# Kernel tuning notes

Hardware: AMD Instinct MI355X
Metric: run time of the kernel (lower is better)

## Reference

```python
import jax, jax.numpy as jnp
import numpy as np

VOCAB = 32000
HID = 1024
HEADS = 16
HEAD_DIM = HID // HEADS
LAYERS = 8
INTER = 4 * HID
ROPE_BASE = 100000.0
EPS = 1e-5


def setup_inputs() -> dict:
    key = jax.random.key(0)
    ks = jax.random.split(key, 12)
    s = 0.02
    inp = {
        'input_ids': jax.random.randint(ks[0], (2, 2048), 0, VOCAB),
        'embed_W': jax.random.normal(ks[1], (VOCAB, HID), jnp.float32) * s,
        'Wq': jax.random.normal(ks[2], (LAYERS, HID, HID), jnp.float32) * s,
        'Wk': jax.random.normal(ks[3], (LAYERS, HID, HID), jnp.float32) * s,
        'Wv': jax.random.normal(ks[4], (LAYERS, HID, HID), jnp.float32) * s,
        'Wo': jax.random.normal(ks[5], (LAYERS, HID, HID), jnp.float32) * s,
        'Wg': jax.random.normal(ks[6], (LAYERS, HID, INTER), jnp.float32) * s,
        'Wu': jax.random.normal(ks[7], (LAYERS, HID, INTER), jnp.float32) * s,
        'Wd': jax.random.normal(ks[8], (LAYERS, INTER, HID), jnp.float32) * s,
        'norm1_w': jnp.ones((LAYERS, HID), jnp.float32),
        'norm2_w': jnp.ones((LAYERS, HID), jnp.float32),
        'final_norm_w': jnp.ones((HID,), jnp.float32),
        'head_W': jax.random.normal(ks[9], (HID, VOCAB), jnp.float32) * s,
    }
    return inp


def rms_norm(x, w):
    return x * jax.lax.rsqrt(jnp.mean(x * x, axis=-1, keepdims=True) + EPS) * w


def rope_tables(seq_len):
    freq = 1.0 / (ROPE_BASE ** (jnp.arange(0, HEAD_DIM, 2, dtype=jnp.float32) / HEAD_DIM))
    ang = jnp.arange(seq_len, dtype=jnp.float32)[:, None] * freq  # [S, d/2]
    cos = jnp.concatenate([jnp.cos(ang), jnp.cos(ang)], axis=-1)  # [S, d]
    sin = jnp.concatenate([jnp.sin(ang), jnp.sin(ang)], axis=-1)
    return cos, sin


def rotate_half(x):
    h = x.shape[-1] // 2
    return jnp.concatenate([-x[..., h:], x[..., :h]], axis=-1)


def apply_rope(q, k, cos, sin):
    # q,k: [B,S,H,D]; cos,sin: [S,D] -> broadcast over heads via [:,None,:]
    c = cos[:, None, :]
    s = sin[:, None, :]
    return q * c + rotate_half(q) * s, k * c + rotate_half(k) * s


def attention(x, wq, wk, wv, wo, cos, sin, causal_mask):
    B, S, _ = x.shape
    q = (x @ wq).reshape(B, S, HEADS, HEAD_DIM)
    k = (x @ wk).reshape(B, S, HEADS, HEAD_DIM)
    v = (x @ wv).reshape(B, S, HEADS, HEAD_DIM)
    q, k = apply_rope(q, k, cos, sin)
    scores = jnp.einsum('bqhd,bkhd->bhqk', q, k) / np.sqrt(HEAD_DIM)
    scores = jnp.clip(scores, -1000.0, 1000.0)
    scores = jnp.where(causal_mask, jnp.finfo(scores.dtype).min, scores)
    w = jax.nn.softmax(scores.astype(jnp.float32), axis=-1).astype(q.dtype)
    w = jnp.clip(w, 0.0, 1.0)
    ctx = jnp.einsum('bhqk,bkhd->bqhd', w, v).reshape(B, S, HID)
    return ctx @ wo


def reference(input_ids, embed_W, Wq, Wk, Wv, Wo, Wg, Wu, Wd, norm1_w, norm2_w, final_norm_w, head_W):
    B, S = input_ids.shape
    h = embed_W[input_ids]  # [B,S,HID]
    cos, sin = rope_tables(S)
    causal_mask = jnp.triu(jnp.ones((S, S), bool), k=1)[None, None]
    for l in range(LAYERS):
        h = h + attention(rms_norm(h, norm1_w[l]), Wq[l], Wk[l], Wv[l], Wo[l], cos, sin, causal_mask)
        hn = rms_norm(h, norm2_w[l])
        h = h + (jax.nn.silu(hn @ Wg[l]) * (hn @ Wu[l])) @ Wd[l]
    h = rms_norm(h, final_norm_w)
    logits = h @ head_W
    return logits, h
```

## Files before the change

kernel.cpp:

```cpp
#include <hip/hip_runtime.h>

#define T_TOK 4096
#define SEQ   2048
#define HID   1024
#define NH    16
#define HD    64
#define INTER 4096
#define NLAYER 8
#define VOCAB 32000

typedef short short8 __attribute__((ext_vector_type(8)));
typedef float f32x4  __attribute__((ext_vector_type(4)));

__device__ __forceinline__ unsigned short f2bf(float f){
  unsigned int u = __builtin_bit_cast(unsigned int, f);
  u += 0x7fffu + ((u >> 16) & 1u);
  return (unsigned short)(u >> 16);
}
__device__ __forceinline__ float bf2f(unsigned short b){
  unsigned int u = ((unsigned int)b) << 16;
  return __builtin_bit_cast(float, u);
}

#define GLOAD_LDS16(gsrc, ldst) \
  __builtin_amdgcn_global_load_lds((const __attribute__((address_space(1))) void*)(gsrc), \
                                   (__attribute__((address_space(3))) void*)(ldst), 16, 0, 0)

__global__ __launch_bounds__(256) void embed_kernel(const int* __restrict__ ids,
                                                    const float* __restrict__ W,
                                                    float* __restrict__ h){
  int i = blockIdx.x * 256 + threadIdx.x;
  int t = i >> 8, c = i & 255;
  ((float4*)h)[i] = ((const float4*)(W + (size_t)ids[t] * HID))[c];
}

__global__ __launch_bounds__(256) void rope_tab_kernel(float* __restrict__ cosT,
                                                       float* __restrict__ sinT){
  int i = blockIdx.x * 256 + threadIdx.x;
  int s = i >> 5, f = i & 31;
  float inv = expf(-((2.0f * (float)f) / 64.0f) * logf(100000.0f));
  float ang = (float)s * inv;
  cosT[i] = cosf(ang);
  sinT[i] = sinf(ang);
}

__global__ __launch_bounds__(256) void rmsnorm_kernel(const float* __restrict__ h,
                                                      const float* __restrict__ w,
                                                      unsigned short* __restrict__ out,
                                                      float* hcopy){
  int t = blockIdx.x, tid = threadIdx.x;
  float4 v = ((const float4*)(h + (size_t)t * HID))[tid];
  float ss = v.x*v.x + v.y*v.y + v.z*v.z + v.w*v.w;
  #pragma unroll
  for (int m = 1; m < 64; m <<= 1) ss += __shfl_xor(ss, m);
  __shared__ float red[4];
  if ((tid & 63) == 0) red[tid >> 6] = ss;
  __syncthreads();
  float r = rsqrtf((red[0] + red[1] + red[2] + red[3]) * (1.0f / HID) + 1e-5f);
  float4 wv = ((const float4*)w)[tid];
  float nx = v.x * r * wv.x;
  float ny = v.y * r * wv.y;
  float nz = v.z * r * wv.z;
  float nw = v.w * r * wv.w;
  ushort4 o;
  o.x = f2bf(nx); o.y = f2bf(ny); o.z = f2bf(nz); o.w = f2bf(nw);
  ((ushort4*)(out + (size_t)t * HID))[tid] = o;
  if (hcopy){
    float4 hv; hv.x = nx; hv.y = ny; hv.z = nz; hv.w = nw;
    ((float4*)(hcopy + (size_t)t * HID))[tid] = hv;
  }
}

__global__ __launch_bounds__(256) void convert_w_swz(const float* __restrict__ W,
                                                     unsigned short* __restrict__ Wt,
                                                     int K, int N){
  __shared__ unsigned short t_lds[64][72];
  W  += (size_t)blockIdx.z * K * N;
  Wt += (size_t)blockIdx.z * K * N;
  const int n0 = blockIdx.x * 64, k0 = blockIdx.y * 64;
  const int tid = threadIdx.x;
  const int tr = tid >> 4, tc = tid & 15;
  #pragma unroll
  for (int i = 0; i < 4; ++i){
    int kk = tr + i * 16;
    float4 v = *(const float4*)(W + (size_t)(k0 + kk) * N + n0 + tc * 4);
    t_lds[tc*4+0][kk] = f2bf(v.x);
    t_lds[tc*4+1][kk] = f2bf(v.y);
    t_lds[tc*4+2][kk] = f2bf(v.z);
    t_lds[tc*4+3][kk] = f2bf(v.w);
  }
  __syncthreads();
  const int n = tid >> 2, cp = tid & 3;
  #pragma unroll
  for (int j = 0; j < 2; ++j){
    int c = cp * 2 + j;
    uint4 d = *(const uint4*)(&t_lds[n][c * 8]);
    *(uint4*)(Wt + (size_t)(n0 + n) * K + k0 + ((c ^ (n & 7)) << 3)) = d;
  }
}

__global__ __launch_bounds__(256) void convert_w_lin(const float* __restrict__ W,
                                                     unsigned short* __restrict__ Wt,
                                                     int K, int N){
  __shared__ unsigned short t_lds[64][72];
  const int n0 = blockIdx.x * 64, k0 = blockIdx.y * 64;
  const int tid = threadIdx.x;
  const int tr = tid >> 4, tc = tid & 15;
  #pragma unroll
  for (int i = 0; i < 4; ++i){
    int kk = tr + i * 16;
    float4 v = *(const float4*)(W + (size_t)(k0 + kk) * N + n0 + tc * 4);
    t_lds[tc*4+0][kk] = f2bf(v.x);
    t_lds[tc*4+1][kk] = f2bf(v.y);
    t_lds[tc*4+2][kk] = f2bf(v.z);
    t_lds[tc*4+3][kk] = f2bf(v.w);
  }
  __syncthreads();
  const int n = tid >> 2, cp = tid & 3;
  #pragma unroll
  for (int j = 0; j < 2; ++j){
    int c = cp * 2 + j;
    uint4 d = *(const uint4*)(&t_lds[n][c * 8]);
    *(uint4*)(Wt + (size_t)(n0 + n) * K + k0 + c * 8) = d;
  }
}

__device__ __forceinline__ void gemm_core64(const unsigned short* __restrict__ A,
                                            const unsigned short* __restrict__ Bt,
                                            int K, int m0, int n0,
                                            unsigned short* As, unsigned short* Bs,
                                            f32x4 (&acc)[4][4]){
  const int tid = threadIdx.x;
  const int lane = tid & 63, w = tid >> 6;
  const int l15 = lane & 15, g = lane >> 4;
  const int lr = lane >> 3;
  const int lc = lane & 7;
  const int wr = w >> 1, wc = w & 1;
  const int axor = ((lc ^ lr) << 3);

  #pragma unroll
  for (int m = 0; m < 4; ++m)
    #pragma unroll
    for (int n = 0; n < 4; ++n)
      #pragma unroll
      for (int i = 0; i < 4; ++i) acc[m][n][i] = 0.0f;

  for (int kk = 0; kk < K; kk += 64){
    __syncthreads();
    #pragma unroll
    for (int i = 0; i < 4; ++i){
      int rb = (i * 4 + w) * 8;
      GLOAD_LDS16(A  + (size_t)(m0 + rb + lr) * K + kk + axor,      As + rb * 64);
      GLOAD_LDS16(Bt + (size_t)(n0 + rb + lr) * K + kk + (lc << 3), Bs + rb * 64);
    }
    __syncthreads();
    short8 a[4][2], b[4][2];
    const int x = l15 & 7;
    #pragma unroll
    for (int m = 0; m < 4; ++m){
      int row = wr * 64 + m * 16 + l15;
      a[m][0] = *(const short8*)(As + row * 64 + ((g       ^ x) << 3));
      a[m][1] = *(const short8*)(As + row * 64 + (((4 + g) ^ x) << 3));
    }
    #pragma unroll
    for (int n = 0; n < 4; ++n){
      int row = wc * 64 + n * 16 + l15;
      b[n][0] = *(const short8*)(Bs + row * 64 + ((g       ^ x) << 3));
      b[n][1] = *(const short8*)(Bs + row * 64 + (((4 + g) ^ x) << 3));
    }
    #pragma unroll
    for (int m = 0; m < 4; ++m)
      #pragma unroll
      for (int n = 0; n < 4; ++n){
        acc[m][n] = __builtin_amdgcn_mfma_f32_16x16x32_bf16(a[m][0], b[n][0], acc[m][n], 0, 0, 0);
        acc[m][n] = __builtin_amdgcn_mfma_f32_16x16x32_bf16(a[m][1], b[n][1], acc[m][n], 0, 0, 0);
      }
  }
}

__device__ __forceinline__ void gemm_core32(const unsigned short* __restrict__ A,
                                            const unsigned short* __restrict__ Bt,
                                            int K, int m0, int n0,
                                            unsigned short* As, unsigned short* Bs,
                                            f32x4 (&acc)[4][4]){
  const int tid = threadIdx.x;
  const int lane = tid & 63, w = tid >> 6;
  const int l15 = lane & 15, g = lane >> 4;
  const int wr = w >> 1, wc = w & 1;
  const int srow = lane >> 2;
  const int schunk = (((lane & 3) ^ ((srow >> 1) & 3)) << 3);
  const int sx = (l15 >> 1) & 3;

  #pragma unroll
  for (int m = 0; m < 4; ++m)
    #pragma unroll
    for (int n = 0; n < 4; ++n)
      #pragma unroll
      for (int i = 0; i < 4; ++i) acc[m][n][i] = 0.0f;

  for (int kk = 0; kk < K; kk += 32){
    __syncthreads();
    GLOAD_LDS16(A  + (size_t)(m0 +      w*16 + srow) * K + kk + schunk, As + (w*16) * 32);
    GLOAD_LDS16(A  + (size_t)(m0 + 64 + w*16 + srow) * K + kk + schunk, As + (64 + w*16) * 32);
    GLOAD_LDS16(Bt + (size_t)(n0 +      w*16 + srow) * K + kk + schunk, Bs + (w*16) * 32);
    GLOAD_LDS16(Bt + (size_t)(n0 + 64 + w*16 + srow) * K + kk + schunk, Bs + (64 + w*16) * 32);
    __syncthreads();
    short8 a[4], b[4];
    #pragma unroll
    for (int m = 0; m < 4; ++m)
      a[m] = *(const short8*)(As + (wr*64 + m*16 + l15) * 32 + ((g ^ sx) << 3));
    #pragma unroll
    for (int n = 0; n < 4; ++n)
      b[n] = *(const short8*)(Bs + (wc*64 + n*16 + l15) * 32 + ((g ^ sx) << 3));
    #pragma unroll
    for (int m = 0; m < 4; ++m)
      #pragma unroll
      for (int n = 0; n < 4; ++n)
        acc[m][n] = __builtin_amdgcn_mfma_f32_16x16x32_bf16(a[m], b[n], acc[m][n], 0, 0, 0);
  }
}

template<int MODE>
__device__ __forceinline__ void gemm_epi(const f32x4 (&acc)[4][4], void* Cout,
                                         const float* __restrict__ resid,
                                         int N, int m0, int n0, int ldt){
  const int tid = threadIdx.x;
  const int lane = tid & 63, w = tid >> 6;
  const int l15 = lane & 15, g = lane >> 4;
  const int wr = w >> 1, wc = w & 1;
  #pragma unroll
  for (int m = 0; m < 4; ++m){
    #pragma unroll
    for (int n = 0; n < 4; ++n){
      int row0 = m0 + wr * 64 + m * 16 + g * 4;
      int col  = n0 + wc * 64 + n * 16 + l15;
      #pragma unroll
      for (int i = 0; i < 4; ++i){
        float v = acc[m][n][i];
        if (MODE == 0){
          ((unsigned short*)Cout)[(size_t)(row0 + i) * N + col] = f2bf(v);
        } else if (MODE == 1){
          size_t idx = (size_t)(row0 + i) * N + col;
          ((float*)Cout)[idx] = resid[idx] + v;
        } else if (MODE == 2){
          ((unsigned short*)Cout)[(size_t)col * ldt + (row0 + i)] = f2bf(v);
        } else {
          __builtin_nontemporal_store(v, &((float*)Cout)[(size_t)(row0 + i) * N + col]);
        }
      }
    }
  }
}

template<int MODE>
__global__ __launch_bounds__(256) void gemm64_k(const unsigned short* __restrict__ A,
                                                const unsigned short* __restrict__ Bt,
                                                void* Cout, const float* resid,
                                                int K, int N, int ldt){
  __shared__ unsigned short As[128 * 64];
  __shared__ unsigned short Bs[128 * 64];
  f32x4 acc[4][4];
  gemm_core64(A, Bt, K, blockIdx.x * 128, blockIdx.y * 128, As, Bs, acc);
  gemm_epi<MODE>(acc, Cout, resid, N, blockIdx.x * 128, blockIdx.y * 128, ldt);
}

template<int MODE>
__global__ __launch_bounds__(256) void gemm32_k(const unsigned short* __restrict__ A,
                                                const unsigned short* __restrict__ Bt,
                                                void* Cout, const float* resid,
                                                int K, int N, int ldt){
  __shared__ unsigned short As[128 * 32];
  __shared__ unsigned short Bs[128 * 32];
  f32x4 acc[4][4];
  gemm_core32(A, Bt, K, blockIdx.x * 128, blockIdx.y * 128, As, Bs, acc);
  gemm_epi<MODE>(acc, Cout, resid, N, blockIdx.x * 128, blockIdx.y * 128, ldt);
}

__global__ __launch_bounds__(256) void gemm_qkv(const unsigned short* __restrict__ A,
                                                const unsigned short* __restrict__ BtQ,
                                                const unsigned short* __restrict__ BtK,
                                                const unsigned short* __restrict__ BtV,
                                                unsigned short* qb, unsigned short* kb,
                                                unsigned short* vt,
                                                const float* __restrict__ cosT,
                                                const float* __restrict__ sinT){
  __shared__ unsigned short As[128 * 64];
  __shared__ unsigned short Bs[128 * 64];
  const int nb = blockIdx.y, sel = nb >> 3, n0 = (nb & 7) * 128;
  const unsigned short* Bt = (sel == 0) ? BtQ : (sel == 1) ? BtK : BtV;
  f32x4 acc[4][4];
  gemm_core64(A, Bt, HID, blockIdx.x * 128, n0, As, Bs, acc);
  if (sel == 2){
    gemm_epi<2>(acc, vt, nullptr, HID, blockIdx.x * 128, n0, T_TOK);
    return;
  }
  unsigned short* outp = sel ? kb : qb;
  const float qs = sel ? 1.0f : 0.125f;
  const int tid = threadIdx.x;
  const int lane = tid & 63, w = tid >> 6;
  const int l15 = lane & 15, g = lane >> 4;
  const int wr = w >> 1, wc = w & 1;
  const int m0 = blockIdx.x * 128;
  #pragma unroll
  for (int m = 0; m < 4; ++m){
    #pragma unroll
    for (int n = 0; n < 2; ++n){
      int row0 = m0 + wr * 64 + m * 16 + g * 4;
      int col  = n0 + wc * 64 + n * 16 + l15;
      int f    = (col & 63);
      #pragma unroll
      for (int i = 0; i < 4; ++i){
        int t = row0 + i, s = t & (SEQ - 1);
        float c  = cosT[s * 32 + f];
        float sn = sinT[s * 32 + f];
        float x0 = acc[m][n][i], x1 = acc[m][n + 2][i];
        outp[(size_t)t * HID + col]      = f2bf((x0 * c - x1 * sn) * qs);
        outp[(size_t)t * HID + col + 32] = f2bf((x1 * c + x0 * sn) * qs);
      }
    }
  }
}

__global__ __launch_bounds__(256) void gemm_gu(const unsigned short* __restrict__ A,
                                               const unsigned short* __restrict__ BtG,
                                               const unsigned short* __restrict__ BtU,
                                               unsigned short* gb, unsigned short* ub){
  __shared__ unsigned short As[128 * 64];
  __shared__ unsigned short Bs[128 * 64];
  const int nb = blockIdx.y, sel = nb >> 5, n0 = (nb & 31) * 128;
  f32x4 acc[4][4];
  gemm_core64(A, sel ? BtU : BtG, HID, blockIdx.x * 128, n0, As, Bs, acc);
  gemm_epi<0>(acc, sel ? ub : gb, nullptr, INTER, blockIdx.x * 128, n0, 0);
}

__global__ __launch_bounds__(256, 2) void gemm_f32b(const unsigned short* __restrict__ A,
                                                    const float* __restrict__ Bw,
                                                    float* __restrict__ Cout,
                                                    int M, int N, int K){
  __shared__ unsigned short As[128 * 32];
  __shared__ unsigned short Bs[128 * 32];
  const int tid = threadIdx.x;
  const int lane = tid & 63, wid = tid >> 6;
  const int l15 = lane & 15, g = lane >> 4;
  const int wr = wid >> 1, wc = wid & 1;
  const int m0 = blockIdx.x * 128, n0 = blockIdx.y * 128;
  const int bcol = tid & 127, bhalf = tid >> 7;
  f32x4 acc[4][4];
  #pragma unroll
  for (int m = 0; m < 4; ++m)
    #pragma unroll
    for (int n = 0; n < 4; ++n)
      #pragma unroll
      for (int i = 0; i < 4; ++i) acc[m][n][i] = 0.0f;
  for (int kk = 0; kk < K; kk += 32){
    __syncthreads();
    #pragma unroll
    for (int cc = 0; cc < 2; ++cc){
      int c = tid + cc * 256;
      int row = c >> 2, kc = (c & 3) << 3;
      uint4 d = *(const uint4*)(A + (size_t)(m0 + row) * K + kk + kc);
      *(uint4*)(&As[row * 32 + kc]) = d;
    }
    {
      const float* bp = Bw + (size_t)(kk + bhalf * 16) * N + n0 + bcol;
      float f[16];
      #pragma unroll
      for (int j = 0; j < 16; ++j) f[j] = bp[(size_t)j * N];
      unsigned int pk[8];
      #pragma unroll
      for (int j = 0; j < 8; ++j)
        pk[j] = (unsigned int)f2bf(f[2*j]) | ((unsigned int)f2bf(f[2*j+1]) << 16);
      int sw = (bcol >> 1) & 3;
      int c0 = ((bhalf << 1)     ) ^ sw;
      int c1 = ((bhalf << 1) | 1 ) ^ sw;
      uint4 w0; w0.x = pk[0]; w0.y = pk[1]; w0.z = pk[2]; w0.w = pk[3];
      uint4 w1; w1.x = pk[4]; w1.y = pk[5]; w1.z = pk[6]; w1.w = pk[7];
      *(uint4*)(&Bs[bcol * 32 + c0 * 8]) = w0;
      *(uint4*)(&Bs[bcol * 32 + c1 * 8]) = w1;
    }
    __syncthreads();
    short8 a[4], b[4];
    #pragma unroll
    for (int m = 0; m < 4; ++m)
      a[m] = *(const short8*)(&As[(wr*64 + m*16 + l15) * 32 + g*8]);
    #pragma unroll
    for (int n = 0; n < 4; ++n){
      int col = wc*64 + n*16 + l15;
      b[n] = *(const short8*)(&Bs[col * 32 + (g ^ ((col >> 1) & 3)) * 8]);
    }
    #pragma unroll
    for (int m = 0; m < 4; ++m)
      #pragma unroll
      for (int n = 0; n < 4; ++n)
        acc[m][n] = __builtin_amdgcn_mfma_f32_16x16x32_bf16(a[m], b[n], acc[m][n], 0, 0, 0);
  }
  #pragma unroll
  for (int m = 0; m < 4; ++m)
    #pragma unroll
    for (int n = 0; n < 4; ++n){
      int row0 = m0 + wr*64 + m*16 + g*4;
      int col  = n0 + wc*64 + n*16 + l15;
      #pragma unroll
      for (int i = 0; i < 4; ++i)
        Cout[(size_t)(row0 + i) * N + col] = acc[m][n][i];
    }
}

__global__ __launch_bounds__(512) void attn_kernel(const unsigned short* __restrict__ q,
                                                   const unsigned short* __restrict__ k,
                                                   const unsigned short* __restrict__ vt,
                                                   unsigned short* __restrict__ ctx){
  const int tid = threadIdx.x;
  const int lane = tid & 63, w = tid >> 6;
  const int l15 = lane & 15, g = lane >> 4;
  const int bx = (int)gridDim.x - 1 - (int)blockIdx.x;
  const int q0 = bx * 128 + w * 16;
  const int hh = blockIdx.y;
  const int tb = blockIdx.z * SEQ;

  __shared__ unsigned short Ks[64][72];
  __shared__ unsigned short Vs[64][72];
  __shared__ unsigned short Ps[8][16][72];

  short8 qa[2];
  #pragma unroll
  for (int kd = 0; kd < 2; ++kd)
    qa[kd] = *(const short8*)(q + (size_t)(tb + q0 + l15) * HID + hh*HD + kd*32 + g*8);

  float m_run[4], l_run[4];
  f32x4 o_acc[4];
  #pragma unroll
  for (int i = 0; i < 4; ++i){ m_run[i] = -1e30f; l_run[i] = 0.0f; }
  #pragma unroll
  for (int dt = 0; dt < 4; ++dt)
    #pragma unroll
    for (int i = 0; i < 4; ++i) o_acc[dt][i] = 0.0f;

  const int ntile = 2 * bx + 2;
  const int srow = tid >> 3, sc = (tid & 7) * 8;
  const unsigned short* kbase = k  + (size_t)(tb + srow) * HID + hh*HD + sc;
  const unsigned short* vbase = vt + (size_t)(hh*HD + srow) * T_TOK + tb + sc;

  for (int kt = 0; kt < ntile; ++kt){
    const int kv0 = kt * 64;
    __syncthreads();
    *(uint4*)(&Ks[srow][sc]) = *(const uint4*)(kbase + (size_t)kv0 * HID);
    *(uint4*)(&Vs[srow][sc]) = *(const uint4*)(vbase + kv0);
    __syncthreads();
    const int dq = q0 + 15 - kv0;
    const int nct = (dq < 0) ? 0 : min(4, (dq >> 4) + 1);
    if (nct <= 0) continue;

    float pv[4][4];
    #pragma unroll
    for (int ct = 0; ct < 4; ++ct){
      if (ct < nct){
        f32x4 scv;
        #pragma unroll
        for (int i = 0; i < 4; ++i) scv[i] = 0.0f;
        scv = __builtin_amdgcn_mfma_f32_16x16x32_bf16(qa[0],
                *(const short8*)(&Ks[ct*16 + l15][g*8]), scv, 0, 0, 0);
        scv = __builtin_amdgcn_mfma_f32_16x16x32_bf16(qa[1],
                *(const short8*)(&Ks[ct*16 + l15][32 + g*8]), scv, 0, 0, 0);
        #pragma unroll
        for (int i = 0; i < 4; ++i){
          float s = fminf(fmaxf(scv[i], -1000.0f), 1000.0f);
          int row = q0 + g*4 + i;
          int col = kv0 + ct*16 + l15;
          pv[ct][i] = (col > row) ? -1e30f : s;
        }
      } else {
        #pragma unroll
        for (int i = 0; i < 4; ++i) pv[ct][i] = -1e30f;
      }
    }
    #pragma unroll
    for (int i = 0; i < 4; ++i){
      float mx = fmaxf(fmaxf(pv[0][i], pv[1][i]), fmaxf(pv[2][i], pv[3][i]));
      #pragma unroll
      for (int msk = 1; msk < 16; msk <<= 1) mx = fmaxf(mx, __shfl_xor(mx, msk));
      if (!__all(mx <= m_run[i] + 8.0f)){
        float mnew = fmaxf(m_run[i], mx);
        float scale = __expf(m_run[i] - mnew);
        m_run[i] = mnew;
        l_run[i] *= scale;
        #pragma unroll
        for (int dt = 0; dt < 4; ++dt) o_acc[dt][i] *= scale;
      }
      float psum = 0.0f;
      #pragma unroll
      for (int ct = 0; ct < 4; ++ct){
        if (ct < nct){
          float p = __expf(pv[ct][i] - m_run[i]);
          pv[ct][i] = p; psum += p;
        } else pv[ct][i] = 0.0f;
      }
      #pragma unroll
      for (int msk = 1; msk < 16; msk <<= 1) psum += __shfl_xor(psum, msk);
      l_run[i] += psum;
    }
    #pragma unroll
    for (int ct = 0; ct < 4; ++ct)
      #pragma unroll
      for (int i = 0; i < 4; ++i)
        Ps[w][g*4 + i][ct*16 + l15] = f2bf(pv[ct][i]);
    const int nks = (nct + 1) >> 1;
    #pragma unroll
    for (int ks = 0; ks < 2; ++ks){
      if (ks < nks){
        short8 ap = *(const short8*)(&Ps[w][l15][ks*32 + g*8]);
        #pragma unroll
        for (int dt = 0; dt < 4; ++dt){
          short8 vb = *(const short8*)(&Vs[dt*16 + l15][ks*32 + g*8]);
          o_acc[dt] = __builtin_amdgcn_mfma_f32_16x16x32_bf16(ap, vb, o_acc[dt], 0, 0, 0);
        }
      }
    }
  }
  #pragma unroll
  for (int dt = 0; dt < 4; ++dt)
    #pragma unroll
    for (int i = 0; i < 4; ++i){
      float o = o_acc[dt][i] / l_run[i];
      ctx[(size_t)(tb + q0 + g*4 + i) * HID + hh*HD + dt*16 + l15] = f2bf(o);
    }
}

__global__ __launch_bounds__(256) void silu_mul_kernel(unsigned short* __restrict__ gbuf,
                                                       const unsigned short* __restrict__ ubuf){
  int i = blockIdx.x * 256 + threadIdx.x;
  short8 gv = ((const short8*)gbuf)[i];
  short8 uv = ((const short8*)ubuf)[i];
  short8 o;
  #pragma unroll
  for (int j = 0; j < 8; ++j){
    float x = bf2f((unsigned short)gv[j]);
    float u = bf2f((unsigned short)uv[j]);
    o[j] = (short)f2bf((x / (1.0f + __expf(-x))) * u);
  }
  ((short8*)gbuf)[i] = o;
}

extern "C" void kernel_launch(void* const* d_in, const int* in_sizes, int n_in,
                              void* d_out, int out_size, void* d_ws, size_t ws_size,
                              hipStream_t stream){
  const int*   ids    = (const int*)d_in[0];
  const float* embedW = (const float*)d_in[1];
  const float* Wq = (const float*)d_in[2];
  const float* Wk = (const float*)d_in[3];
  const float* Wv = (const float*)d_in[4];
  const float* Wo = (const float*)d_in[5];
  const float* Wg = (const float*)d_in[6];
  const float* Wu = (const float*)d_in[7];
  const float* Wd = (const float*)d_in[8];
  const float* n1 = (const float*)d_in[9];
  const float* n2 = (const float*)d_in[10];
  const float* nf = (const float*)d_in[11];
  const float* Wh = (const float*)d_in[12];
  float* out = (float*)d_out;

  char* scb = (char*)d_out;
  unsigned short* qb  = (unsigned short*)(scb + 0);
  unsigned short* kb  = (unsigned short*)(scb + 8388608);
  unsigned short* vtb = (unsigned short*)(scb + 16777216);
  unsigned short* ctx = (unsigned short*)(scb + 25165824);
  unsigned short* gb  = (unsigned short*)(scb + 33554432);
  unsigned short* ub  = (unsigned short*)(scb + 67108864);
  float* cosT = (float*)(scb + 100663296);
  float* sinT = (float*)(scb + 100925440);
  float* h_fallback   = (float*)(scb + 104857600);
  unsigned short* WtQ = (unsigned short*)(scb + 134217728);
  unsigned short* WtK = (unsigned short*)(scb + 150994944);
  unsigned short* WtV = (unsigned short*)(scb + 167772160);
  unsigned short* WtO = (unsigned short*)(scb + 184549376);
  unsigned short* WtG = (unsigned short*)(scb + 201326592);
  unsigned short* WtU = (unsigned short*)(scb + 268435456);
  unsigned short* WtD = (unsigned short*)(scb + 335544320);

  unsigned short* xn = (unsigned short*)d_ws;
  float* h = (ws_size >= 25165824u) ? (float*)((char*)d_ws + 8388608) : h_fallback;
  unsigned short* WhT = (ws_size >= 90701824u)
                      ? (unsigned short*)((char*)d_ws + 25165824) : nullptr;

  convert_w_swz<<<dim3(16, 16, 8), 256, 0, stream>>>(Wq, WtQ, HID, HID);
  convert_w_swz<<<dim3(16, 16, 8), 256, 0, stream>>>(Wk, WtK, HID, HID);
  convert_w_swz<<<dim3(16, 16, 8), 256, 0, stream>>>(Wv, WtV, HID, HID);
  convert_w_swz<<<dim3(16, 16, 8), 256, 0, stream>>>(Wo, WtO, HID, HID);
  convert_w_swz<<<dim3(64, 16, 8), 256, 0, stream>>>(Wg, WtG, HID, INTER);
  convert_w_swz<<<dim3(64, 16, 8), 256, 0, stream>>>(Wu, WtU, HID, INTER);
  convert_w_swz<<<dim3(16, 64, 8), 256, 0, stream>>>(Wd, WtD, INTER, HID);
  if (WhT)
    convert_w_lin<<<dim3(500, 16, 1), 256, 0, stream>>>(Wh, WhT, HID, VOCAB);

  embed_kernel<<<4096, 256, 0, stream>>>(ids, embedW, h);
  rope_tab_kernel<<<256, 256, 0, stream>>>(cosT, sinT);

  for (int l = 0; l < NLAYER; ++l){
    rmsnorm_kernel<<<4096, 256, 0, stream>>>(h, n1 + l*HID, xn, nullptr);
    gemm_qkv<<<dim3(32, 24), 256, 0, stream>>>(xn, WtQ + (size_t)l*HID*HID,
                                               WtK + (size_t)l*HID*HID,
                                               WtV + (size_t)l*HID*HID, qb, kb, vtb,
                                               cosT, sinT);
    attn_kernel<<<dim3(16, 16, 2), 512, 0, stream>>>(qb, kb, vtb, ctx);
    gemm64_k<1><<<dim3(32, 8), 256, 0, stream>>>(ctx, WtO + (size_t)l*HID*HID,
                                                 h, h, HID, HID, 0);
    rmsnorm_kernel<<<4096, 256, 0, stream>>>(h, n2 + l*HID, xn, nullptr);
    gemm_gu<<<dim3(32, 64), 256, 0, stream>>>(xn, WtG + (size_t)l*HID*INTER,
                                              WtU + (size_t)l*HID*INTER, gb, ub);
    silu_mul_kernel<<<8192, 256, 0, stream>>>(gb, ub);
    gemm64_k<1><<<dim3(32, 8), 256, 0, stream>>>(gb, WtD + (size_t)l*HID*INTER,
                                                 h, h, INTER, HID, 0);
  }

  rmsnorm_kernel<<<4096, 256, 0, stream>>>(h, nf, xn, out + 131072000);
  if (WhT)
    gemm32_k<3><<<dim3(32, 250), 256, 0, stream>>>(xn, WhT, out, nullptr, HID, VOCAB, 0);
  else
    gemm_f32b<<<dim3(32, 250), 256, 0, stream>>>(xn, Wh, out, T_TOK, VOCAB, HID);
}
```

Measured before the change: 3.879 ms.

## Fuse gate/up GEMMs with SiLU-multiply epilogue and merge QKVO weight conversion

The gate and up projections now run in the same workgroup back to back. The gate accumulator is kept packed as bf16 in registers, and the SiLU(g)*u product is written straight out. This removes the separate silu_mul kernel and the round trip of the up buffer through memory. The four QKVO weight-conversion launches are also merged into one launch over 32 z-slices. The trade-offs are half as many GEMM blocks, each doing twice the work, higher register pressure from holding the gate results, and rounding the gate values to bf16 before SiLU as the old code already did.

```diff
diff --git a/kernel.cpp b/kernel.cpp
--- a/kernel.cpp
+++ b/kernel.cpp
@@ -68,6 +68,38 @@
   if (hcopy){
     float4 hv; hv.x = nx; hv.y = ny; hv.z = nz; hv.w = nw;
     ((float4*)(hcopy + (size_t)t * HID))[tid] = hv;
+  }
+}
+
+__global__ __launch_bounds__(256) void convert_w_qkvo(const float* __restrict__ W0,
+                                                      const float* __restrict__ W1,
+                                                      const float* __restrict__ W2,
+                                                      const float* __restrict__ W3,
+                                                      unsigned short* __restrict__ Wt){
+  __shared__ unsigned short t_lds[64][72];
+  const int z = blockIdx.z, sel = z >> 3, l = z & 7;
+  const float* W = ((sel == 0) ? W0 : (sel == 1) ? W1 : (sel == 2) ? W2 : W3)
+                 + (size_t)l * HID * HID;
+  unsigned short* dst = Wt + (size_t)z * HID * HID;
+  const int n0 = blockIdx.x * 64, k0 = blockIdx.y * 64;
+  const int tid = threadIdx.x;
+  const int tr = tid >> 4, tc = tid & 15;
+  #pragma unroll
+  for (int i = 0; i < 4; ++i){
+    int kk = tr + i * 16;
+    float4 v = *(const float4*)(W + (size_t)(k0 + kk) * HID + n0 + tc * 4);
+    t_lds[tc*4+0][kk] = f2bf(v.x);
+    t_lds[tc*4+1][kk] = f2bf(v.y);
+    t_lds[tc*4+2][kk] = f2bf(v.z);
+    t_lds[tc*4+3][kk] = f2bf(v.w);
+  }
+  __syncthreads();
+  const int n = tid >> 2, cp = tid & 3;
+  #pragma unroll
+  for (int j = 0; j < 2; ++j){
+    int c = cp * 2 + j;
+    uint4 d = *(const uint4*)(&t_lds[n][c * 8]);
+    *(uint4*)(dst + (size_t)(n0 + n) * HID + k0 + ((c ^ (n & 7)) << 3)) = d;
   }
 }
 
@@ -321,16 +353,43 @@
   }
 }
 
-__global__ __launch_bounds__(256) void gemm_gu(const unsigned short* __restrict__ A,
-                                               const unsigned short* __restrict__ BtG,
-                                               const unsigned short* __restrict__ BtU,
-                                               unsigned short* gb, unsigned short* ub){
+__global__ __launch_bounds__(256) void gemm_gusilu(const unsigned short* __restrict__ A,
+                                                   const unsigned short* __restrict__ BtG,
+                                                   const unsigned short* __restrict__ BtU,
+                                                   unsigned short* __restrict__ gb){
   __shared__ unsigned short As[128 * 64];
   __shared__ unsigned short Bs[128 * 64];
-  const int nb = blockIdx.y, sel = nb >> 5, n0 = (nb & 31) * 128;
+  const int m0 = blockIdx.x * 128, n0 = blockIdx.y * 128;
   f32x4 acc[4][4];
-  gemm_core64(A, sel ? BtU : BtG, HID, blockIdx.x * 128, n0, As, Bs, acc);
-  gemm_epi<0>(acc, sel ? ub : gb, nullptr, INTER, blockIdx.x * 128, n0, 0);
+  gemm_core64(A, BtG, HID, m0, n0, As, Bs, acc);
+  unsigned int gp[4][4][2];
+  #pragma unroll
+  for (int m = 0; m < 4; ++m)
+    #pragma unroll
+    for (int n = 0; n < 4; ++n){
+      gp[m][n][0] = (unsigned int)f2bf(acc[m][n][0]) | ((unsigned int)f2bf(acc[m][n][1]) << 16);
+      gp[m][n][1] = (unsigned int)f2bf(acc[m][n][2]) | ((unsigned int)f2bf(acc[m][n][3]) << 16);
+    }
+  gemm_core64(A, BtU, HID, m0, n0, As, Bs, acc);
+  const int tid = threadIdx.x;
+  const int lane = tid & 63, w = tid >> 6;
+  const int l15 = lane & 15, g = lane >> 4;
+  const int wr = w >> 1, wc = w & 1;
+  #pragma unroll
+  for (int m = 0; m < 4; ++m){
+    #pragma unroll
+    for (int n = 0; n < 4; ++n){
+      int row0 = m0 + wr * 64 + m * 16 + g * 4;
+      int col  = n0 + wc * 64 + n * 16 + l15;
+      #pragma unroll
+      for (int i = 0; i < 4; ++i){
+        float gv = bf2f((unsigned short)(gp[m][n][i >> 1] >> ((i & 1) * 16)));
+        float u  = acc[m][n][i];
+        float s  = (gv / (1.0f + __expf(-gv))) * u;
+        gb[(size_t)(row0 + i) * INTER + col] = f2bf(s);
+      }
+    }
+  }
 }
 
 __global__ __launch_bounds__(256, 2) void gemm_f32b(const unsigned short* __restrict__ A,
@@ -526,21 +585,6 @@
     }
 }
 
-__global__ __launch_bounds__(256) void silu_mul_kernel(unsigned short* __restrict__ gbuf,
-                                                       const unsigned short* __restrict__ ubuf){
-  int i = blockIdx.x * 256 + threadIdx.x;
-  short8 gv = ((const short8*)gbuf)[i];
-  short8 uv = ((const short8*)ubuf)[i];
-  short8 o;
-  #pragma unroll
-  for (int j = 0; j < 8; ++j){
-    float x = bf2f((unsigned short)gv[j]);
-    float u = bf2f((unsigned short)uv[j]);
-    o[j] = (short)f2bf((x / (1.0f + __expf(-x))) * u);
-  }
-  ((short8*)gbuf)[i] = o;
-}
-
 extern "C" void kernel_launch(void* const* d_in, const int* in_sizes, int n_in,
                               void* d_out, int out_size, void* d_ws, size_t ws_size,
                               hipStream_t stream){
@@ -565,7 +609,6 @@
   unsigned short* vtb = (unsigned short*)(scb + 16777216);
   unsigned short* ctx = (unsigned short*)(scb + 25165824);
   unsigned short* gb  = (unsigned short*)(scb + 33554432);
-  unsigned short* ub  = (unsigned short*)(scb + 67108864);
   float* cosT = (float*)(scb + 100663296);
   float* sinT = (float*)(scb + 100925440);
   float* h_fallback   = (float*)(scb + 104857600);
@@ -582,10 +625,7 @@
   unsigned short* WhT = (ws_size >= 90701824u)
                       ? (unsigned short*)((char*)d_ws + 25165824) : nullptr;
 
-  convert_w_swz<<<dim3(16, 16, 8), 256, 0, stream>>>(Wq, WtQ, HID, HID);
-  convert_w_swz<<<dim3(16, 16, 8), 256, 0, stream>>>(Wk, WtK, HID, HID);
-  convert_w_swz<<<dim3(16, 16, 8), 256, 0, stream>>>(Wv, WtV, HID, HID);
-  convert_w_swz<<<dim3(16, 16, 8), 256, 0, stream>>>(Wo, WtO, HID, HID);
+  convert_w_qkvo<<<dim3(16, 16, 32), 256, 0, stream>>>(Wq, Wk, Wv, Wo, WtQ);
   convert_w_swz<<<dim3(64, 16, 8), 256, 0, stream>>>(Wg, WtG, HID, INTER);
   convert_w_swz<<<dim3(64, 16, 8), 256, 0, stream>>>(Wu, WtU, HID, INTER);
   convert_w_swz<<<dim3(16, 64, 8), 256, 0, stream>>>(Wd, WtD, INTER, HID);
@@ -605,9 +645,8 @@
     gemm64_k<1><<<dim3(32, 8), 256, 0, stream>>>(ctx, WtO + (size_t)l*HID*HID,
                                                  h, h, HID, HID, 0);
     rmsnorm_kernel<<<4096, 256, 0, stream>>>(h, n2 + l*HID, xn, nullptr);
-    gemm_gu<<<dim3(32, 64), 256, 0, stream>>>(xn, WtG + (size_t)l*HID*INTER,
-                                              WtU + (size_t)l*HID*INTER, gb, ub);
-    silu_mul_kernel<<<8192, 256, 0, stream>>>(gb, ub);
+    gemm_gusilu<<<dim3(32, 32), 256, 0, stream>>>(xn, WtG + (size_t)l*HID*INTER,
+                                                  WtU + (size_t)l*HID*INTER, gb);
     gemm64_k<1><<<dim3(32, 8), 256, 0, stream>>>(gb, WtD + (size_t)l*HID*INTER,
                                                  h, h, INTER, HID, 0);
   }
```

Measured after the change: 3.880 ms. No clear change (+0.0%).
